# Kernel optimization log

Measured on AMD Instinct MI355X. Metric: run time of the kernel, lower is better.

## Reference

```python
import jax, jax.numpy as jnp
import numpy as np

NEG_SLOPE = 0.2
# relation r: src node type SRC[r], dst node type DST[r]; 0=Drug, 1=Disease
# order: TREATS, TREATED_BY, HAS_CONTRAIND, CONTRAIND_BY, HAS_PARENTCODE, HAS_CHILDCODE, INTERACTS
SRC = (0, 1, 0, 1, 1, 1, 0)
DST = (1, 0, 1, 0, 1, 1, 0)

N_DRUG, N_DIS, D_IN, HID, OUT, E = 20000, 40000, 256, 128, 128, 150000


def _gat(x_src, x_dst, edge_index, Ws, Wd, a_s, a_d, b):
    # single-head PyG GATConv, add_self_loops=False
    hs = x_src @ Ws                      # [Ns, H]
    hd = x_dst @ Wd                      # [Nd, H]
    src, dst = edge_index[0], edge_index[1]
    n_dst = x_dst.shape[0]
    alpha_src = hs @ a_s                 # [Ns]
    alpha_dst = hd @ a_d                 # [Nd]
    alpha = jax.nn.leaky_relu(alpha_src[src] + alpha_dst[dst], NEG_SLOPE)  # [E]
    amax = jax.ops.segment_max(alpha, dst, num_segments=n_dst)
    amax = jnp.where(jnp.isfinite(amax), amax, 0.0)
    ex = jnp.exp(alpha - amax[dst])
    denom = jax.ops.segment_sum(ex, dst, num_segments=n_dst)
    coef = ex / (denom[dst] + 1e-16)     # per-destination softmax (PyG softmax)
    out = jax.ops.segment_sum(hs[src] * coef[:, None], dst, num_segments=n_dst)
    return out + b


def _hetero_layer(xd, xi, edges, Ws, Wd, a_s, a_d, b):
    feats = (xd, xi)
    H = b.shape[1]
    outs = [jnp.zeros((xd.shape[0], H), xd.dtype), jnp.zeros((xi.shape[0], H), xi.dtype)]
    for r in range(7):
        o = _gat(feats[SRC[r]], feats[DST[r]], edges[r], Ws[r], Wd[r], a_s[r], a_d[r], b[r])
        outs[DST[r]] = outs[DST[r]] + o   # HeteroConv aggr='sum'
    return outs[0], outs[1]


def setup_inputs() -> dict:
    key = jax.random.key(0)
    ks = jax.random.split(key, 32)
    x_drug = jax.random.normal(ks[0], (N_DRUG, D_IN), jnp.float32)
    x_disease = jax.random.normal(ks[1], (N_DIS, D_IN), jnp.float32)
    nsz = (N_DRUG, N_DIS)
    edges = []
    for r in range(7):
        s = jax.random.randint(ks[2 + 2 * r], (E,), 0, nsz[SRC[r]], jnp.int32)
        d = jax.random.randint(ks[3 + 2 * r], (E,), 0, nsz[DST[r]], jnp.int32)
        edges.append(jnp.stack([s, d]))
    s = 0.1
    W1s = s * jax.random.normal(ks[16], (7, D_IN, HID), jnp.float32)
    W1d = s * jax.random.normal(ks[17], (7, D_IN, HID), jnp.float32)
    W1d = W1d.at[6].set(W1s[6])  # INTERACTS shares src/dst lin (GATConv(-1,...))
    a1s = s * jax.random.normal(ks[18], (7, HID), jnp.float32)
    a1d = s * jax.random.normal(ks[19], (7, HID), jnp.float32)
    b1 = jnp.zeros((7, HID), jnp.float32)
    W2s = s * jax.random.normal(ks[20], (7, HID, HID), jnp.float32)
    W2d = s * jax.random.normal(ks[21], (7, HID, HID), jnp.float32)
    W2d = W2d.at[6].set(W2s[6])
    a2s = s * jax.random.normal(ks[22], (7, HID), jnp.float32)
    a2d = s * jax.random.normal(ks[23], (7, HID), jnp.float32)
    b2 = jnp.zeros((7, HID), jnp.float32)
    W_drug = s * jax.random.normal(ks[24], (HID, OUT), jnp.float32)
    b_drug = jnp.zeros((OUT,), jnp.float32)
    W_dis = s * jax.random.normal(ks[25], (HID, OUT), jnp.float32)
    b_dis = jnp.zeros((OUT,), jnp.float32)
    return {"x_drug": x_drug, "x_disease": x_disease,
            "e_treats": edges[0], "e_treated_by": edges[1], "e_contraind": edges[2],
            "e_contraind_by": edges[3], "e_parent": edges[4], "e_child": edges[5],
            "e_interacts": edges[6],
            "W1s": W1s, "W1d": W1d, "a1s": a1s, "a1d": a1d, "b1": b1,
            "W2s": W2s, "W2d": W2d, "a2s": a2s, "a2d": a2d, "b2": b2,
            "W_drug": W_drug, "b_drug": b_drug, "W_dis": W_dis, "b_dis": b_dis}


def reference(x_drug, x_disease, e_treats, e_treated_by, e_contraind, e_contraind_by,
              e_parent, e_child, e_interacts,
              W1s, W1d, a1s, a1d, b1, W2s, W2d, a2s, a2d, b2,
              W_drug, b_drug, W_dis, b_dis):
    edges = (e_treats, e_treated_by, e_contraind, e_contraind_by, e_parent, e_child, e_interacts)
    xd, xi = _hetero_layer(x_drug, x_disease, edges, W1s, W1d, a1s, a1d, b1)
    xd, xi = jax.nn.relu(xd), jax.nn.relu(xi)  # dropout is identity (eval mode)
    xd, xi = _hetero_layer(xd, xi, edges, W2s, W2d, a2s, a2d, b2)
    out_drug = jax.nn.relu(xd @ W_drug + b_drug)
    out_disease = jax.nn.relu(xi @ W_dis + b_dis)
    return out_drug, out_disease
```

## Files before the change

kernel.cpp:

```cpp
#include <hip/hip_runtime.h>
#include <stdint.h>

#define NDRUG 20000
#define NDIS  40000
#define HID   128
#define NE    150000
#define NREL  7
#define RPSTR (NDIS + 1)
#define NS_TOT (NREL * RPSTR)
#define CPX   ((NE + 255) / 256)

typedef unsigned short ushort_t;
typedef __attribute__((ext_vector_type(8))) short bf16x8;
typedef __attribute__((ext_vector_type(4))) float f32x4;
typedef const __attribute__((address_space(1))) void gv_t;
typedef __attribute__((address_space(3))) void lv_t;

__device__ __forceinline__ ushort_t f2bf(float f) {
  unsigned u = __float_as_uint(f);
  u += 0x7FFFu + ((u >> 16) & 1u);
  return (ushort_t)(u >> 16);
}
__device__ __forceinline__ float bf2f(ushort_t h) {
  return __uint_as_float(((unsigned)h) << 16);
}

struct GemmJob { const ushort_t* A; const ushort_t* BT; const float* bias; void* C; int M, N; };

template<bool BIAS, bool RELU, bool BF16OUT>
__global__ __launch_bounds__(256) void gemm_dual(GemmJob j0, GemmJob j1, int gx0, int K)
{
  __shared__ ushort_t As[2][128 * 32];
  __shared__ ushort_t Bs[2][128 * 32];
  const bool first = blockIdx.x < (unsigned)gx0;
  const GemmJob J = first ? j0 : j1;
  const int bx = first ? blockIdx.x : blockIdx.x - gx0;
  if ((int)blockIdx.y * 128 >= J.N) return;
  const int tid = threadIdx.x;
  const int m0 = bx * 128;
  const int n0 = blockIdx.y * 128;
  const int wave = tid >> 6, lane = tid & 63;
  const int wm = wave & 1, wn = wave >> 1;
  const int l15 = lane & 15, lk = lane >> 4;

  const int rowS = wave * 16 + (lane >> 2);
  const int chunk = (lane & 3) * 8;
  const ushort_t* ga0 = J.A + (size_t)min(m0 + rowS, J.M - 1) * K + chunk;
  const ushort_t* ga1 = J.A + (size_t)min(m0 + rowS + 64, J.M - 1) * K + chunk;
  const ushort_t* gb0 = J.BT + (size_t)(n0 + rowS) * K + chunk;
  const ushort_t* gb1 = J.BT + (size_t)(n0 + rowS + 64) * K + chunk;

#define GEMM_STAGE(buf, koff)                                                              \
  do {                                                                                     \
    __builtin_amdgcn_global_load_lds((gv_t*)(ga0 + (koff)), (lv_t*)(&As[buf][wave * 512]), 16, 0, 0);        \
    __builtin_amdgcn_global_load_lds((gv_t*)(ga1 + (koff)), (lv_t*)(&As[buf][wave * 512 + 2048]), 16, 0, 0); \
    __builtin_amdgcn_global_load_lds((gv_t*)(gb0 + (koff)), (lv_t*)(&Bs[buf][wave * 512]), 16, 0, 0);        \
    __builtin_amdgcn_global_load_lds((gv_t*)(gb1 + (koff)), (lv_t*)(&Bs[buf][wave * 512 + 2048]), 16, 0, 0); \
  } while (0)

  f32x4 acc[4][4] = {};
  const int nt = K >> 5;

  GEMM_STAGE(0, 0);
  __syncthreads();

  for (int t = 0; t < nt; ++t) {
    if (t + 1 < nt) GEMM_STAGE((t + 1) & 1, (t + 1) * 32);
    const ushort_t* Ab = As[t & 1];
    const ushort_t* Bb = Bs[t & 1];
    bf16x8 af[4], bfg[4];
    #pragma unroll
    for (int m = 0; m < 4; ++m)
      af[m] = *reinterpret_cast<const bf16x8*>(&Ab[(wm * 64 + m * 16 + l15) * 32 + lk * 8]);
    #pragma unroll
    for (int n = 0; n < 4; ++n)
      bfg[n] = *reinterpret_cast<const bf16x8*>(&Bb[(wn * 64 + n * 16 + l15) * 32 + lk * 8]);
    #pragma unroll
    for (int m = 0; m < 4; ++m)
      #pragma unroll
      for (int n = 0; n < 4; ++n)
        acc[m][n] = __builtin_amdgcn_mfma_f32_16x16x32_bf16(af[m], bfg[n], acc[m][n], 0, 0, 0);
    __syncthreads();
  }
#undef GEMM_STAGE

  #pragma unroll
  for (int m = 0; m < 4; ++m) {
    int rbase = m0 + wm * 64 + m * 16 + lk * 4;
    #pragma unroll
    for (int n = 0; n < 4; ++n) {
      int col = n0 + wn * 64 + n * 16 + l15;
      float bv = 0.f;
      if (BIAS) bv = J.bias[col];
      #pragma unroll
      for (int j = 0; j < 4; ++j) {
        int row = rbase + j;
        if (row >= J.M) continue;
        float v = acc[m][n][j] + bv;
        if (RELU) v = fmaxf(v, 0.f);
        if (BF16OUT) ((ushort_t*)J.C)[(size_t)row * J.N + col] = f2bf(v);
        else         ((float*)J.C)[(size_t)row * J.N + col] = v;
      }
    }
  }
}

__global__ void build_wcat2(const float* __restrict__ WA, ushort_t* __restrict__ outA,
                            int ncolA, int4 relsA,
                            const float* __restrict__ WB, ushort_t* __restrict__ outB,
                            int ncolB, int4 relsB, int K)
{
  int id = blockIdx.x * 256 + threadIdx.x;
  const float* W; ushort_t* out; int ncol; int4 rels;
  int totA = K * ncolA;
  if (id < totA) { W = WA; out = outA; ncol = ncolA; rels = relsA; }
  else {
    id -= totA;
    if (id >= K * ncolB) return;
    W = WB; out = outB; ncol = ncolB; rels = relsB;
  }
  int k = id / ncol, c = id - k * ncol;
  int rr = (&rels.x)[c >> 7];
  out[(size_t)c * K + k] = f2bf(W[((size_t)rr * K + k) * HID + (c & 127)]);
}

__global__ __launch_bounds__(256) void wvec_kernel(
    const float* __restrict__ Wsrc, const float* __restrict__ as_,
    const float* __restrict__ Wdst, const float* __restrict__ ad_,
    float* __restrict__ wv, int K)
{
  int slot = blockIdx.x;
  int r = slot % NREL;
  const float* W = (slot < NREL ? Wsrc : Wdst) + (size_t)r * K * HID;
  const float* a = (slot < NREL ? as_ : ad_) + r * HID;
  int wave = threadIdx.x >> 6, lane = threadIdx.x & 63;
  int k = blockIdx.y * 4 + wave;
  if (k >= K) return;
  float s = W[(size_t)k * HID + lane] * a[lane]
          + W[(size_t)k * HID + 64 + lane] * a[64 + lane];
  #pragma unroll
  for (int off = 32; off; off >>= 1) s += __shfl_xor(s, off);
  if (lane == 0) wv[slot * 256 + k] = s;
}

__global__ void cvt2_f32_bf16(const float* __restrict__ inA, ushort_t* __restrict__ outA, int n8A,
                              const float* __restrict__ inB, ushort_t* __restrict__ outB, int n8B)
{
  int i = blockIdx.x * 256 + threadIdx.x;
  const float* in; ushort_t* out;
  if (i < n8A) { in = inA; out = outA; }
  else {
    i -= n8A;
    if (i >= n8B) return;
    in = inB; out = outB;
  }
  float4 a = reinterpret_cast<const float4*>(in)[2 * i];
  float4 b = reinterpret_cast<const float4*>(in)[2 * i + 1];
  ushort_t r[8] = {f2bf(a.x), f2bf(a.y), f2bf(a.z), f2bf(a.w),
                   f2bf(b.x), f2bf(b.y), f2bf(b.z), f2bf(b.w)};
  reinterpret_cast<uint4*>(out)[i] = *reinterpret_cast<uint4*>(r);
}

struct AlphaJobs { int wslot[8]; int outOff[8]; };

template<int K>
__global__ __launch_bounds__(256) void alpha_dual(
    const ushort_t* __restrict__ XD, const ushort_t* __restrict__ XI,
    const float* __restrict__ wv, float* __restrict__ outBase,
    AlphaJobs jd, AlphaJobs ji, int gbD)
{
  const bool isD = blockIdx.x < (unsigned)gbD;
  const ushort_t* X = isD ? XD : XI;
  const int N = isD ? NDRUG : NDIS;
  const AlphaJobs jobs = isD ? jd : ji;
  int i = (isD ? blockIdx.x : blockIdx.x - gbD) * 256 + threadIdx.x;
  if (i >= N) return;
  float acc[8];
  #pragma unroll
  for (int v = 0; v < 8; ++v) acc[v] = 0.f;
  const ushort_t* xp = X + (size_t)i * K;
  for (int k = 0; k < K; k += 8) {
    uint4 u = *reinterpret_cast<const uint4*>(xp + k);
    unsigned uu[4] = {u.x, u.y, u.z, u.w};
    float xf[8];
    #pragma unroll
    for (int q = 0; q < 4; ++q) {
      xf[2 * q]     = __uint_as_float(uu[q] << 16);
      xf[2 * q + 1] = __uint_as_float(uu[q] & 0xFFFF0000u);
    }
    #pragma unroll
    for (int v = 0; v < 8; ++v) {
      const float* wp = wv + jobs.wslot[v] * 256 + k;
      #pragma unroll
      for (int q = 0; q < 8; ++q) acc[v] += xf[q] * wp[q];
    }
  }
  #pragma unroll
  for (int v = 0; v < 8; ++v) outBase[jobs.outOff[v] + i] = acc[v];
}

struct RelIdx { const int* src[NREL]; const int* dst[NREL]; };
struct NdArr  { int nd[NREL]; };

__global__ void zero_ints(int* __restrict__ p, int n) {
  int i = blockIdx.x * 256 + threadIdx.x;
  if (i < n) p[i] = 0;
}
__global__ void hist_k(RelIdx ri, int* __restrict__ counts) {
  int xcd = blockIdx.x & 7;
  if (xcd >= NREL) return;
  int e = (blockIdx.x >> 3) * 256 + threadIdx.x;
  if (e >= NE) return;
  atomicAdd(&counts[xcd * RPSTR + ri.dst[xcd][e]], 1);
}
__global__ __launch_bounds__(256) void scan_blk(const int* __restrict__ in,
                                                int* __restrict__ partial,
                                                int* __restrict__ bsum, int n)
{
  __shared__ int ts[256];
  int t = threadIdx.x;
  int base = blockIdx.x * 1024 + t * 4;
  int v[4];
  #pragma unroll
  for (int i = 0; i < 4; ++i) v[i] = (base + i < n) ? in[base + i] : 0;
  int s = v[0] + v[1] + v[2] + v[3];
  ts[t] = s; __syncthreads();
  for (int off = 1; off < 256; off <<= 1) {
    int x = (t >= off) ? ts[t - off] : 0;
    __syncthreads();
    ts[t] += x;
    __syncthreads();
  }
  int run = ts[t] - s;
  #pragma unroll
  for (int i = 0; i < 4; ++i) {
    if (base + i < n) partial[base + i] = run;
    run += v[i];
  }
  if (t == 255) bsum[blockIdx.x] = ts[255];
}
__global__ __launch_bounds__(512) void scan_fin(const int* __restrict__ partial,
                                                const int* __restrict__ bsum,
                                                int* __restrict__ rowptr,
                                                int* __restrict__ cursor, int n)
{
  __shared__ int ts[512];
  int t = threadIdx.x;
  ts[t] = (t < (int)blockIdx.x) ? bsum[t] : 0;
  __syncthreads();
  #pragma unroll
  for (int off = 256; off; off >>= 1) {
    if (t < off) ts[t] += ts[t + off];
    __syncthreads();
  }
  int base = ts[0];
  #pragma unroll
  for (int i = 0; i < 2; ++i) {
    int idx = blockIdx.x * 1024 + t + i * 512;
    if (idx < n) {
      int v = partial[idx] + base;
      rowptr[idx] = v; cursor[idx] = v;
    }
  }
}
__global__ void fill_k(RelIdx ri, int* __restrict__ cursor, int* __restrict__ colsrc) {
  int xcd = blockIdx.x & 7;
  if (xcd >= NREL) return;
  int e = (blockIdx.x >> 3) * 256 + threadIdx.x;
  if (e >= NE) return;
  int d = ri.dst[xcd][e];
  int pos = atomicAdd(&cursor[xcd * RPSTR + d], 1);
  colsrc[pos] = ri.src[xcd][e];
}

__global__ __launch_bounds__(256) void coef_k(
    const int* __restrict__ rowptr, const int* __restrict__ colsrc,
    float* __restrict__ coef, const float* __restrict__ alphaB, NdArr nds)
{
  int d = blockIdx.x * 256 + threadIdx.x;
  int r = blockIdx.y;
  if (d >= nds.nd[r]) return;
  int beg = rowptr[r * RPSTR + d], end = rowptr[r * RPSTR + d + 1];
  if (beg == end) return;
  const float ad = alphaB[(NREL + r) * NDIS + d];
  const float* as = alphaB + (size_t)r * NDIS;
  int deg = end - beg;
  if (deg <= 16) {
    float av[16];
    float m = -1e30f;
    #pragma unroll
    for (int i = 0; i < 16; ++i) {
      float a = -1e30f;
      if (i < deg) {
        int s = colsrc[beg + i];
        a = as[s] + ad;
        a = a > 0.f ? a : 0.2f * a;
      }
      av[i] = a;
      m = fmaxf(m, a);
    }
    float sum = 0.f;
    #pragma unroll
    for (int i = 0; i < 16; ++i) {
      if (i < deg) {
        float ex = __expf(av[i] - m);
        av[i] = ex;
        sum += ex;
      }
    }
    float inv = 1.f / (sum + 1e-16f);
    #pragma unroll
    for (int i = 0; i < 16; ++i)
      if (i < deg) coef[beg + i] = av[i] * inv;
  } else {
    float m = -1e30f;
    for (int i = beg; i < end; ++i) {
      float a = as[colsrc[i]] + ad;
      a = a > 0.f ? a : 0.2f * a;
      m = fmaxf(m, a);
    }
    float sum = 0.f;
    for (int i = beg; i < end; ++i) {
      float a = as[colsrc[i]] + ad;
      a = a > 0.f ? a : 0.2f * a;
      float ex = __expf(a - m);
      coef[i] = ex;
      sum += ex;
    }
    float inv = 1.f / (sum + 1e-16f);
    for (int i = beg; i < end; ++i) coef[i] *= inv;
  }
}

struct PvRel { int rel; int rowptr_off; const ushort_t* hs; int hst; int hoff; };
struct PvParams { PvRel dr[3]; PvRel di[4]; };

template<bool RELU>
__global__ __launch_bounds__(256) void pv_multi(
    PvParams P, const int* __restrict__ rowptr, const int* __restrict__ colsrc,
    const float* __restrict__ coef, const float* __restrict__ bias,
    ushort_t* __restrict__ outD, ushort_t* __restrict__ outI, int nbD)
{
  const int wave = threadIdx.x >> 6, lane = threadIdx.x & 63;
  const int c0 = 2 * lane;
  const bool isD = blockIdx.x < (unsigned)nbD;
  const int d = (isD ? blockIdx.x : blockIdx.x - nbD) * 4 + wave;
  const int Nd = isD ? NDRUG : NDIS;
  if (d >= Nd) return;
  const int nr = isD ? 3 : 4;
  float acc0 = 0.f, acc1 = 0.f;

  #pragma unroll
  for (int q = 0; q < 4; ++q) {
    if (q >= nr) break;
    const PvRel R = isD ? P.dr[q] : P.di[q];
    acc0 += bias[R.rel * HID + c0];
    acc1 += bias[R.rel * HID + c0 + 1];
    const int beg = rowptr[R.rowptr_off + d];
    const int end = rowptr[R.rowptr_off + d + 1];
    if (beg == end) continue;
    const ushort_t* hsb = R.hs + R.hoff + c0;
    const int hst = R.hst;
    for (int c = beg; c < end; c += 4) {
      float cf[4]; int si[4];
      #pragma unroll
      for (int j = 0; j < 4; ++j) {
        int idx = (c + j < end) ? c + j : end - 1;
        cf[j] = (c + j < end) ? coef[idx] : 0.f;
        si[j] = colsrc[idx];
      }
      ushort2 hv[4];
      #pragma unroll
      for (int j = 0; j < 4; ++j)
        hv[j] = *reinterpret_cast<const ushort2*>(hsb + (size_t)si[j] * hst);
      #pragma unroll
      for (int j = 0; j < 4; ++j) {
        acc0 += cf[j] * bf2f(hv[j].x);
        acc1 += cf[j] * bf2f(hv[j].y);
      }
    }
  }
  if (RELU) { acc0 = fmaxf(acc0, 0.f); acc1 = fmaxf(acc1, 0.f); }
  ushort2 o; o.x = f2bf(acc0); o.y = f2bf(acc1);
  ushort_t* out = isD ? outD : outI;
  *reinterpret_cast<ushort2*>(out + (size_t)d * HID + c0) = o;
}

static const int DSTh[NREL] = {1, 0, 1, 0, 1, 1, 0};

struct WsPlan {
  ushort_t *xdb1, *xib1, *xd1b, *xi1b, *xd2b, *xi2b;
  ushort_t *hs_d, *hs_i, *wcatT_d, *wcatT_i, *wfinT_d, *wfinT_i;
  float *alphaB, *wv, *coef;
  int *counts, *rowptr, *cursor, *colsrc, *bsum;
  size_t total_bytes;
};

static WsPlan plan_ws(void* d_ws) {
  WsPlan p;
  ushort_t* s = (ushort_t*)d_ws;
  p.xdb1 = s;     s += (size_t)NDRUG * 256;
  p.xib1 = s;     s += (size_t)NDIS * 256;
  p.xd1b = s;     s += (size_t)NDRUG * HID;
  p.xi1b = s;     s += (size_t)NDIS * HID;
  p.hs_d = s;     s += (size_t)NDRUG * 384;
  p.hs_i = s;     s += (size_t)NDIS * 512;
  p.wcatT_d = s;  s += 384 * 256;
  p.wcatT_i = s;  s += 512 * 256;
  p.wfinT_d = s;  s += 128 * 128;
  p.wfinT_i = s;  s += 128 * 128;
  p.xd2b = p.xdb1;
  p.xi2b = p.xib1;
  float* f = (float*)s;
  p.alphaB = f;   f += (size_t)15 * NDIS;
  p.wv = f;       f += 14 * 256;
  p.coef = f;     f += (size_t)NREL * NE;
  int* q = (int*)f;
  p.counts = q;   q += NS_TOT;
  p.rowptr = q;   q += NS_TOT;
  p.cursor = q;   q += NS_TOT;
  p.colsrc = q;   q += NREL * NE;
  p.bsum = q;     q += 512;
  p.total_bytes = (size_t)((char*)q - (char*)d_ws);
  return p;
}

static void run_layer(const ushort_t* XDb, const ushort_t* XIb, int K,
                      const float* Wsrc, const float* Wdst,
                      const float* as_, const float* ad_, const float* bias,
                      ushort_t* outDb, ushort_t* outIb, bool relu,
                      const WsPlan& p, hipStream_t stream)
{
  int4 rd = make_int4(0, 2, 6, 0);
  int4 ri4 = make_int4(1, 3, 4, 5);
  build_wcat2<<<(K * 896 + 255) / 256, 256, 0, stream>>>(
      Wsrc, p.wcatT_d, 384, rd, Wsrc, p.wcatT_i, 512, ri4, K);
  wvec_kernel<<<dim3(14, K / 4), 256, 0, stream>>>(Wsrc, as_, Wdst, ad_, p.wv, K);

  AlphaJobs jd = {};
  jd.wslot[0] = 0;     jd.outOff[0] = 0 * NDIS;
  jd.wslot[1] = 2;     jd.outOff[1] = 2 * NDIS;
  jd.wslot[2] = 6;     jd.outOff[2] = 6 * NDIS;
  jd.wslot[3] = 7 + 1; jd.outOff[3] = (7 + 1) * NDIS;
  jd.wslot[4] = 7 + 3; jd.outOff[4] = (7 + 3) * NDIS;
  jd.wslot[5] = 7 + 6; jd.outOff[5] = (7 + 6) * NDIS;
  jd.wslot[6] = 0;     jd.outOff[6] = 14 * NDIS;
  jd.wslot[7] = 0;     jd.outOff[7] = 14 * NDIS;
  AlphaJobs ji = {};
  ji.wslot[0] = 1;     ji.outOff[0] = 1 * NDIS;
  ji.wslot[1] = 3;     ji.outOff[1] = 3 * NDIS;
  ji.wslot[2] = 4;     ji.outOff[2] = 4 * NDIS;
  ji.wslot[3] = 5;     ji.outOff[3] = 5 * NDIS;
  ji.wslot[4] = 7 + 0; ji.outOff[4] = (7 + 0) * NDIS;
  ji.wslot[5] = 7 + 2; ji.outOff[5] = (7 + 2) * NDIS;
  ji.wslot[6] = 7 + 4; ji.outOff[6] = (7 + 4) * NDIS;
  ji.wslot[7] = 7 + 5; ji.outOff[7] = (7 + 5) * NDIS;
  int gbD = (NDRUG + 255) / 256, gbI = (NDIS + 255) / 256;
  if (K == 256)
    alpha_dual<256><<<gbD + gbI, 256, 0, stream>>>(XDb, XIb, p.wv, p.alphaB, jd, ji, gbD);
  else
    alpha_dual<128><<<gbD + gbI, 256, 0, stream>>>(XDb, XIb, p.wv, p.alphaB, jd, ji, gbD);

  GemmJob g0 = {XDb, p.wcatT_d, nullptr, p.hs_d, NDRUG, 384};
  GemmJob g1 = {XIb, p.wcatT_i, nullptr, p.hs_i, NDIS, 512};
  int gx0 = (NDRUG + 127) / 128, gx1 = (NDIS + 127) / 128;
  gemm_dual<false, false, true><<<dim3(gx0 + gx1, 4), 256, 0, stream>>>(g0, g1, gx0, K);

  NdArr nds;
  for (int r = 0; r < NREL; ++r) nds.nd[r] = DSTh[r] == 0 ? NDRUG : NDIS;
  coef_k<<<dim3((NDIS + 255) / 256, NREL), 256, 0, stream>>>(
      p.rowptr, p.colsrc, p.coef, p.alphaB, nds);

  PvParams P;
  P.dr[0] = {1, 1 * RPSTR, p.hs_i, 512, 0};
  P.dr[1] = {3, 3 * RPSTR, p.hs_i, 512, 128};
  P.dr[2] = {6, 6 * RPSTR, p.hs_d, 384, 256};
  P.di[0] = {0, 0 * RPSTR, p.hs_d, 384, 0};
  P.di[1] = {2, 2 * RPSTR, p.hs_d, 384, 128};
  P.di[2] = {4, 4 * RPSTR, p.hs_i, 512, 256};
  P.di[3] = {5, 5 * RPSTR, p.hs_i, 512, 384};
  int nbD = (NDRUG + 3) / 4, nbI = (NDIS + 3) / 4;
  if (relu)
    pv_multi<true><<<nbD + nbI, 256, 0, stream>>>(
        P, p.rowptr, p.colsrc, p.coef, bias, outDb, outIb, nbD);
  else
    pv_multi<false><<<nbD + nbI, 256, 0, stream>>>(
        P, p.rowptr, p.colsrc, p.coef, bias, outDb, outIb, nbD);
}

extern "C" void kernel_launch(void* const* d_in, const int* in_sizes, int n_in,
                              void* d_out, int out_size, void* d_ws, size_t ws_size,
                              hipStream_t stream) {
  const float* x_drug = (const float*)d_in[0];
  const float* x_dis  = (const float*)d_in[1];
  RelIdx ri;
  for (int r = 0; r < NREL; ++r) {
    const int* e = (const int*)d_in[2 + r];
    ri.src[r] = e; ri.dst[r] = e + NE;
  }
  const float* W1s = (const float*)d_in[9];
  const float* W1d = (const float*)d_in[10];
  const float* a1s = (const float*)d_in[11];
  const float* a1d = (const float*)d_in[12];
  const float* b1  = (const float*)d_in[13];
  const float* W2s = (const float*)d_in[14];
  const float* W2d = (const float*)d_in[15];
  const float* a2s = (const float*)d_in[16];
  const float* a2d = (const float*)d_in[17];
  const float* b2  = (const float*)d_in[18];
  const float* Wdr = (const float*)d_in[19];
  const float* bdr = (const float*)d_in[20];
  const float* Wdi = (const float*)d_in[21];
  const float* bdi = (const float*)d_in[22];

  WsPlan p = plan_ws(d_ws);
  if (p.total_bytes > ws_size) return;

  cvt2_f32_bf16<<<((NDRUG + NDIS) * 256 / 8 + 255) / 256, 256, 0, stream>>>(
      x_drug, p.xdb1, NDRUG * 256 / 8, x_dis, p.xib1, NDIS * 256 / 8);

  zero_ints<<<(NS_TOT + 255) / 256, 256, 0, stream>>>(p.counts, NS_TOT);
  hist_k<<<8 * CPX, 256, 0, stream>>>(ri, p.counts);
  int nb = (NS_TOT + 1023) / 1024;
  scan_blk<<<nb, 256, 0, stream>>>(p.counts, p.cursor, p.bsum, NS_TOT);
  scan_fin<<<nb, 512, 0, stream>>>(p.cursor, p.bsum, p.rowptr, p.cursor, NS_TOT);
  fill_k<<<8 * CPX, 256, 0, stream>>>(ri, p.cursor, p.colsrc);

  run_layer(p.xdb1, p.xib1, 256, W1s, W1d, a1s, a1d, b1, p.xd1b, p.xi1b, true, p, stream);
  run_layer(p.xd1b, p.xi1b, 128, W2s, W2d, a2s, a2d, b2, p.xd2b, p.xi2b, false, p, stream);

  int4 r0 = make_int4(0, 0, 0, 0);
  build_wcat2<<<(128 * 128 * 2 + 255) / 256, 256, 0, stream>>>(
      Wdr, p.wfinT_d, 128, r0, Wdi, p.wfinT_i, 128, r0, 128);
  float* out = (float*)d_out;
  GemmJob f0 = {p.xd2b, p.wfinT_d, bdr, out, NDRUG, 128};
  GemmJob f1 = {p.xi2b, p.wfinT_i, bdi, out + (size_t)NDRUG * HID, NDIS, 128};
  int gx0 = (NDRUG + 127) / 128, gx1 = (NDIS + 127) / 128;
  gemm_dual<true, true, false><<<dim3(gx0 + gx1, 1), 256, 0, stream>>>(f0, f1, gx0, 128);
}
```

Before: 451.9 us.

## Fuse per-destination edge softmax into aggregation kernel using wave shuffles

Removes the separate coef_k kernel and its coefficient buffer. Each wave now computes the leaky-relu scores, max, exp-sum and normalized coefficients for its destination's edges with wave-wide shuffle reductions, then broadcasts index and coefficient per edge during the gather. This saves one launch per layer plus the coefficient write and reread, and spreads the softmax across lanes instead of one thread per node. Rows longer than 64 edges fall back to a strided three-pass loop. The zero-fill kernel is also swapped for hipMemsetAsync.

```diff
diff --git a/kernel.cpp b/kernel.cpp
--- a/kernel.cpp
+++ b/kernel.cpp
@@ -200,12 +200,7 @@
 }
 
 struct RelIdx { const int* src[NREL]; const int* dst[NREL]; };
-struct NdArr  { int nd[NREL]; };
-
-__global__ void zero_ints(int* __restrict__ p, int n) {
-  int i = blockIdx.x * 256 + threadIdx.x;
-  if (i < n) p[i] = 0;
-}
+
 __global__ void hist_k(RelIdx ri, int* __restrict__ counts) {
   int xcd = blockIdx.x & 7;
   if (xcd >= NREL) return;
@@ -273,72 +268,14 @@
   colsrc[pos] = ri.src[xcd][e];
 }
 
-__global__ __launch_bounds__(256) void coef_k(
-    const int* __restrict__ rowptr, const int* __restrict__ colsrc,
-    float* __restrict__ coef, const float* __restrict__ alphaB, NdArr nds)
-{
-  int d = blockIdx.x * 256 + threadIdx.x;
-  int r = blockIdx.y;
-  if (d >= nds.nd[r]) return;
-  int beg = rowptr[r * RPSTR + d], end = rowptr[r * RPSTR + d + 1];
-  if (beg == end) return;
-  const float ad = alphaB[(NREL + r) * NDIS + d];
-  const float* as = alphaB + (size_t)r * NDIS;
-  int deg = end - beg;
-  if (deg <= 16) {
-    float av[16];
-    float m = -1e30f;
-    #pragma unroll
-    for (int i = 0; i < 16; ++i) {
-      float a = -1e30f;
-      if (i < deg) {
-        int s = colsrc[beg + i];
-        a = as[s] + ad;
-        a = a > 0.f ? a : 0.2f * a;
-      }
-      av[i] = a;
-      m = fmaxf(m, a);
-    }
-    float sum = 0.f;
-    #pragma unroll
-    for (int i = 0; i < 16; ++i) {
-      if (i < deg) {
-        float ex = __expf(av[i] - m);
-        av[i] = ex;
-        sum += ex;
-      }
-    }
-    float inv = 1.f / (sum + 1e-16f);
-    #pragma unroll
-    for (int i = 0; i < 16; ++i)
-      if (i < deg) coef[beg + i] = av[i] * inv;
-  } else {
-    float m = -1e30f;
-    for (int i = beg; i < end; ++i) {
-      float a = as[colsrc[i]] + ad;
-      a = a > 0.f ? a : 0.2f * a;
-      m = fmaxf(m, a);
-    }
-    float sum = 0.f;
-    for (int i = beg; i < end; ++i) {
-      float a = as[colsrc[i]] + ad;
-      a = a > 0.f ? a : 0.2f * a;
-      float ex = __expf(a - m);
-      coef[i] = ex;
-      sum += ex;
-    }
-    float inv = 1.f / (sum + 1e-16f);
-    for (int i = beg; i < end; ++i) coef[i] *= inv;
-  }
-}
-
-struct PvRel { int rel; int rowptr_off; const ushort_t* hs; int hst; int hoff; };
+struct PvRel { int rel; int rowptr_off; int as_off; int ad_off;
+               const ushort_t* hs; int hst; int hoff; };
 struct PvParams { PvRel dr[3]; PvRel di[4]; };
 
 template<bool RELU>
 __global__ __launch_bounds__(256) void pv_multi(
     PvParams P, const int* __restrict__ rowptr, const int* __restrict__ colsrc,
-    const float* __restrict__ coef, const float* __restrict__ bias,
+    const float* __restrict__ alphaB, const float* __restrict__ bias,
     ushort_t* __restrict__ outD, ushort_t* __restrict__ outI, int nbD)
 {
   const int wave = threadIdx.x >> 6, lane = threadIdx.x & 63;
@@ -358,25 +295,92 @@
     acc1 += bias[R.rel * HID + c0 + 1];
     const int beg = rowptr[R.rowptr_off + d];
     const int end = rowptr[R.rowptr_off + d + 1];
-    if (beg == end) continue;
+    const int deg = end - beg;
+    if (deg == 0) continue;
+    const float ad = alphaB[R.ad_off + d];
+    const float* as = alphaB + R.as_off;
     const ushort_t* hsb = R.hs + R.hoff + c0;
     const int hst = R.hst;
-    for (int c = beg; c < end; c += 4) {
-      float cf[4]; int si[4];
-      #pragma unroll
-      for (int j = 0; j < 4; ++j) {
-        int idx = (c + j < end) ? c + j : end - 1;
-        cf[j] = (c + j < end) ? coef[idx] : 0.f;
-        si[j] = colsrc[idx];
+
+    if (deg <= 64) {
+      int s = 0; float a = -1e30f;
+      if (lane < deg) {
+        s = colsrc[beg + lane];
+        float t = as[s] + ad;
+        a = t > 0.f ? t : 0.2f * t;
       }
-      ushort2 hv[4];
-      #pragma unroll
-      for (int j = 0; j < 4; ++j)
-        hv[j] = *reinterpret_cast<const ushort2*>(hsb + (size_t)si[j] * hst);
-      #pragma unroll
-      for (int j = 0; j < 4; ++j) {
-        acc0 += cf[j] * bf2f(hv[j].x);
-        acc1 += cf[j] * bf2f(hv[j].y);
+      float m = a;
+      #pragma unroll
+      for (int off = 32; off; off >>= 1) m = fmaxf(m, __shfl_xor(m, off));
+      float ex = (lane < deg) ? __expf(a - m) : 0.f;
+      float sum = ex;
+      #pragma unroll
+      for (int off = 32; off; off >>= 1) sum += __shfl_xor(sum, off);
+      const float cn = ex * (1.f / (sum + 1e-16f));
+
+      for (int c = 0; c < deg; c += 4) {
+        float cf[4]; int si[4];
+        #pragma unroll
+        for (int j = 0; j < 4; ++j) {
+          int idx = c + j;
+          cf[j] = (idx < deg) ? __shfl(cn, idx & 63) : 0.f;
+          si[j] = __shfl(s, idx & 63);
+        }
+        ushort2 hv[4];
+        #pragma unroll
+        for (int j = 0; j < 4; ++j)
+          hv[j] = *reinterpret_cast<const ushort2*>(hsb + (size_t)si[j] * hst);
+        #pragma unroll
+        for (int j = 0; j < 4; ++j) {
+          acc0 += cf[j] * bf2f(hv[j].x);
+          acc1 += cf[j] * bf2f(hv[j].y);
+        }
+      }
+    } else {
+      float m = -1e30f;
+      for (int i = beg + lane; i < end; i += 64) {
+        float t = as[colsrc[i]] + ad;
+        t = t > 0.f ? t : 0.2f * t;
+        m = fmaxf(m, t);
+      }
+      #pragma unroll
+      for (int off = 32; off; off >>= 1) m = fmaxf(m, __shfl_xor(m, off));
+      float sum = 0.f;
+      for (int i = beg + lane; i < end; i += 64) {
+        float t = as[colsrc[i]] + ad;
+        t = t > 0.f ? t : 0.2f * t;
+        sum += __expf(t - m);
+      }
+      #pragma unroll
+      for (int off = 32; off; off >>= 1) sum += __shfl_xor(sum, off);
+      const float inv = 1.f / (sum + 1e-16f);
+      for (int cb = beg; cb < end; cb += 64) {
+        int n = min(64, end - cb);
+        int s = 0; float cn = 0.f;
+        if (lane < n) {
+          s = colsrc[cb + lane];
+          float t = as[s] + ad;
+          t = t > 0.f ? t : 0.2f * t;
+          cn = __expf(t - m) * inv;
+        }
+        for (int c = 0; c < n; c += 4) {
+          float cf[4]; int si[4];
+          #pragma unroll
+          for (int j = 0; j < 4; ++j) {
+            int idx = c + j;
+            cf[j] = (idx < n) ? __shfl(cn, idx & 63) : 0.f;
+            si[j] = __shfl(s, idx & 63);
+          }
+          ushort2 hv[4];
+          #pragma unroll
+          for (int j = 0; j < 4; ++j)
+            hv[j] = *reinterpret_cast<const ushort2*>(hsb + (size_t)si[j] * hst);
+          #pragma unroll
+          for (int j = 0; j < 4; ++j) {
+            acc0 += cf[j] * bf2f(hv[j].x);
+            acc1 += cf[j] * bf2f(hv[j].y);
+          }
+        }
       }
     }
   }
@@ -391,7 +395,7 @@
 struct WsPlan {
   ushort_t *xdb1, *xib1, *xd1b, *xi1b, *xd2b, *xi2b;
   ushort_t *hs_d, *hs_i, *wcatT_d, *wcatT_i, *wfinT_d, *wfinT_i;
-  float *alphaB, *wv, *coef;
+  float *alphaB, *wv;
   int *counts, *rowptr, *cursor, *colsrc, *bsum;
   size_t total_bytes;
 };
@@ -414,7 +418,6 @@
   float* f = (float*)s;
   p.alphaB = f;   f += (size_t)15 * NDIS;
   p.wv = f;       f += 14 * 256;
-  p.coef = f;     f += (size_t)NREL * NE;
   int* q = (int*)f;
   p.counts = q;   q += NS_TOT;
   p.rowptr = q;   q += NS_TOT;
@@ -466,26 +469,21 @@
   int gx0 = (NDRUG + 127) / 128, gx1 = (NDIS + 127) / 128;
   gemm_dual<false, false, true><<<dim3(gx0 + gx1, 4), 256, 0, stream>>>(g0, g1, gx0, K);
 
-  NdArr nds;
-  for (int r = 0; r < NREL; ++r) nds.nd[r] = DSTh[r] == 0 ? NDRUG : NDIS;
-  coef_k<<<dim3((NDIS + 255) / 256, NREL), 256, 0, stream>>>(
-      p.rowptr, p.colsrc, p.coef, p.alphaB, nds);
-
   PvParams P;
-  P.dr[0] = {1, 1 * RPSTR, p.hs_i, 512, 0};
-  P.dr[1] = {3, 3 * RPSTR, p.hs_i, 512, 128};
-  P.dr[2] = {6, 6 * RPSTR, p.hs_d, 384, 256};
-  P.di[0] = {0, 0 * RPSTR, p.hs_d, 384, 0};
-  P.di[1] = {2, 2 * RPSTR, p.hs_d, 384, 128};
-  P.di[2] = {4, 4 * RPSTR, p.hs_i, 512, 256};
-  P.di[3] = {5, 5 * RPSTR, p.hs_i, 512, 384};
+  P.dr[0] = {1, 1 * RPSTR, 1 * NDIS, (NREL + 1) * NDIS, p.hs_i, 512, 0};
+  P.dr[1] = {3, 3 * RPSTR, 3 * NDIS, (NREL + 3) * NDIS, p.hs_i, 512, 128};
+  P.dr[2] = {6, 6 * RPSTR, 6 * NDIS, (NREL + 6) * NDIS, p.hs_d, 384, 256};
+  P.di[0] = {0, 0 * RPSTR, 0 * NDIS, (NREL + 0) * NDIS, p.hs_d, 384, 0};
+  P.di[1] = {2, 2 * RPSTR, 2 * NDIS, (NREL + 2) * NDIS, p.hs_d, 384, 128};
+  P.di[2] = {4, 4 * RPSTR, 4 * NDIS, (NREL + 4) * NDIS, p.hs_i, 512, 256};
+  P.di[3] = {5, 5 * RPSTR, 5 * NDIS, (NREL + 5) * NDIS, p.hs_i, 512, 384};
   int nbD = (NDRUG + 3) / 4, nbI = (NDIS + 3) / 4;
   if (relu)
     pv_multi<true><<<nbD + nbI, 256, 0, stream>>>(
-        P, p.rowptr, p.colsrc, p.coef, bias, outDb, outIb, nbD);
+        P, p.rowptr, p.colsrc, p.alphaB, bias, outDb, outIb, nbD);
   else
     pv_multi<false><<<nbD + nbI, 256, 0, stream>>>(
-        P, p.rowptr, p.colsrc, p.coef, bias, outDb, outIb, nbD);
+        P, p.rowptr, p.colsrc, p.alphaB, bias, outDb, outIb, nbD);
 }
 
 extern "C" void kernel_launch(void* const* d_in, const int* in_sizes, int n_in,
@@ -519,7 +517,7 @@
   cvt2_f32_bf16<<<((NDRUG + NDIS) * 256 / 8 + 255) / 256, 256, 0, stream>>>(
       x_drug, p.xdb1, NDRUG * 256 / 8, x_dis, p.xib1, NDIS * 256 / 8);
 
-  zero_ints<<<(NS_TOT + 255) / 256, 256, 0, stream>>>(p.counts, NS_TOT);
+  hipMemsetAsync(p.counts, 0, NS_TOT * sizeof(int), stream);
   hist_k<<<8 * CPX, 256, 0, stream>>>(ri, p.counts);
   int nb = (NS_TOT + 1023) / 1024;
   scan_blk<<<nb, 256, 0, stream>>>(p.counts, p.cursor, p.bsum, NS_TOT);
```

Result: no change. 443.2 us (-1.9%).
